# Performance work log

Measured on AMD Instinct MI355X. Metric: run time of the kernel, lower is better.

The kernel has to match this reference:

```python
import jax, jax.numpy as jnp
import numpy as np

ALPHA = 0.15
KSIZE = 5
EPS = 1e-6


def _minmax_norm(x):
    # x: [B,1,H,W]; per-sample min-max normalize, 0.5 if nearly constant
    mn = x.min(axis=(1, 2, 3), keepdims=True)
    mx = x.max(axis=(1, 2, 3), keepdims=True)
    denom = mx - mn
    safe = jnp.where(denom > EPS, denom, 1.0)
    return jnp.where(denom > EPS, (x - mn) / safe, 0.5)


def _saliency_map(images, out_hw):
    # grayscale via luma weights
    w = jnp.array([0.299, 0.587, 0.114], dtype=images.dtype).reshape(1, 3, 1, 1)
    gray = (images * w).sum(axis=1, keepdims=True)  # [B,1,H,W]
    kernel = jnp.ones((1, 1, KSIZE, KSIZE), dtype=gray.dtype) / (KSIZE * KSIZE)
    dn = ('NCHW', 'OIHW', 'NCHW')
    local_mean = jax.lax.conv_general_dilated(gray, kernel, (1, 1), 'SAME', dimension_numbers=dn)
    local_mean_sq = jax.lax.conv_general_dilated(gray ** 2, kernel, (1, 1), 'SAME', dimension_numbers=dn)
    local_var = jnp.maximum(local_mean_sq - local_mean ** 2, 0.0)
    sal = _minmax_norm(local_var)
    if sal.shape[-2:] != out_hw:
        sal = jax.image.resize(sal, (sal.shape[0], 1, out_hw[0], out_hw[1]), method='bilinear')
    return jax.lax.stop_gradient(sal)  # computed under no_grad / detached in torch


def setup_inputs() -> dict:
    key = jax.random.key(0)
    k1, k2 = jax.random.split(key)
    features = jax.random.normal(k1, (64, 512, 28, 28), dtype=jnp.float32)
    images = jax.random.uniform(k2, (64, 3, 224, 224), dtype=jnp.float32)
    return {"features": features, "images": images}


def reference(features, images):
    sal = _saliency_map(images, features.shape[-2:])  # [B,1,Hf,Wf]
    attn = jnp.sqrt((features ** 2).mean(axis=1, keepdims=True))  # [B,1,Hf,Wf]
    attn = _minmax_norm(attn)
    loss = jnp.mean((attn - sal) ** 2)
    return ALPHA * loss
```

## Files before the change

kernel.cpp:

```cpp
#include <hip/hip_runtime.h>
#include <math.h>

#define BATCH 64
#define HIMG 224
#define WIMG 224
#define IMGPLANE (HIMG*WIMG)
#define CF 512
#define HF 28
#define WF 28
#define POS (HF*WF)
#define ALPHA_C 0.15f
#define EPS_C 1e-6f

#define STRIPS 14
#define SROWS 16
#define GROWS 20
#define GCOLS 228
#define GSTR 229
#define VSTR 261

#define OFF_HRES 0
#define HRES_CNT (BATCH*HIMG*WF)
#define OFF_BMM (OFF_HRES + HRES_CNT)
#define OFF_AP  (OFF_BMM + BATCH*STRIPS*2)
#define OFF_LP  (OFF_AP + 2*BATCH*POS)

__global__ __launch_bounds__(256) void varh_k(const float* __restrict__ img,
                                              float* __restrict__ ws) {
    __shared__ float g[GROWS * GSTR];
    __shared__ float v[SROWS * VSTR];
    __shared__ float wred[8];
    int b = blockIdx.y, sy = blockIdx.x;
    int tid = threadIdx.x;
    int y0 = sy * SROWS;
    const float* imb = img + (size_t)b * 3 * IMGPLANE;

    for (int i = tid; i < GROWS * GCOLS; i += 256) {
        int gr = i / GCOLS, gc = i - gr * GCOLS;
        int gy = y0 - 2 + gr, gx = gc - 2;
        float u = 0.0f;
        if ((unsigned)gy < HIMG && (unsigned)gx < WIMG) {
            int o = gy * WIMG + gx;
            u = 0.299f * imb[o] + 0.587f * imb[IMGPLANE + o] + 0.114f * imb[2 * IMGPLANE + o];
        }
        g[gr * GSTR + gc] = u;
    }
    if (tid < SROWS * 8) {
        int r = tid >> 3, p = tid & 7;
        int jh = p + ((p < 4) ? 0 : 224);
        v[r * VSTR + jh + (jh >> 3)] = 0.0f;
    }
    __syncthreads();

    int r = tid >> 4, s = tid & 15;
    int x0 = 14 * s;
    const float* gr0 = g + r * GSTR;
    float c1[5], c2[5];
    #pragma unroll
    for (int m = 0; m < 5; m++) {
        float a = 0.0f, a2 = 0.0f;
        #pragma unroll
        for (int k = 0; k < 5; k++) {
            float u = gr0[k * GSTR + x0 + m];
            a += u; a2 += u * u;
        }
        c1[m] = a; c2[m] = a2;
    }
    float vmn = INFINITY, vmx = 0.0f;
    #pragma unroll
    for (int xi = 0; xi < 14; xi++) {
        int p = xi % 5;
        float s1 = c1[p], s2 = c2[p];
        #pragma unroll
        for (int m = 1; m < 5; m++) {
            s1 += c1[(p + m) % 5];
            s2 += c2[(p + m) % 5];
        }
        float m1 = s1 * 0.04f, m2 = s2 * 0.04f;
        float vv = fmaxf(m2 - m1 * m1, 0.0f);
        int jh = x0 + xi + 4;
        v[r * VSTR + jh + (jh >> 3)] = vv;
        vmn = fminf(vmn, vv); vmx = fmaxf(vmx, vv);
        if (xi < 13) {
            float a = 0.0f, a2 = 0.0f;
            #pragma unroll
            for (int k = 0; k < 5; k++) {
                float u = gr0[k * GSTR + x0 + xi + 5];
                a += u; a2 += u * u;
            }
            c1[p] = a; c2[p] = a2;
        }
    }
    #pragma unroll
    for (int o = 32; o > 0; o >>= 1) {
        vmn = fminf(vmn, __shfl_xor(vmn, o));
        vmx = fmaxf(vmx, __shfl_xor(vmx, o));
    }
    int w = tid >> 6;
    if ((tid & 63) == 0) { wred[w] = vmn; wred[4 + w] = vmx; }
    __syncthreads();
    if (tid == 0) {
        float mn = fminf(fminf(wred[0], wred[1]), fminf(wred[2], wred[3]));
        float mx = fmaxf(fmaxf(wred[4], wred[5]), fmaxf(wred[6], wred[7]));
        int blk = b * STRIPS + sy;
        ws[OFF_BMM + 2 * blk]     = mn;
        ws[OFF_BMM + 2 * blk + 1] = mx;
    }

    float* hb = ws + OFF_HRES + ((size_t)b * HIMG + y0) * WF;
    for (int idx = tid; idx < SROWS * WF; idx += 256) {
        int rr = idx / WF, i = idx - rr * WF;
        float acc = 0.0f, wsum = 0.0f;
        int j0 = 8 * i - 4;
        #pragma unroll
        for (int t = 0; t < 16; t++) {
            int j = j0 + t;
            float w_ = 8.0f - fabsf((float)t - 7.5f);
            int jh = j + 4;
            acc += w_ * v[rr * VSTR + jh + (jh >> 3)];
            if ((unsigned)j < WIMG) wsum += w_;
        }
        hb[idx] = acc / wsum;
    }
}

__global__ __launch_bounds__(256) void attn_k(const float* __restrict__ f,
                                              float* __restrict__ ws) {
    int p = blockIdx.x * 256 + threadIdx.x;
    int b = blockIdx.y, z = blockIdx.z;
    if (p >= POS) return;
    const float* fp = f + ((size_t)b * CF + (size_t)z * 256) * POS + p;
    float acc = 0.0f;
    #pragma unroll 16
    for (int c = 0; c < 256; c++) {
        float v = fp[(size_t)c * POS];
        acc += v * v;
    }
    ws[OFF_AP + ((size_t)z * BATCH + b) * POS + p] = acc;
}

__global__ __launch_bounds__(256) void fused_k(float* __restrict__ ws) {
    __shared__ float hres[HIMG][WF + 1];
    __shared__ float wred[4];
    __shared__ float s_mn, s_mx;
    int b = blockIdx.x;
    int tid = threadIdx.x;

    if (tid < 64) {
        float mn = INFINITY, mx = 0.0f;
        if (tid < STRIPS) {
            mn = ws[OFF_BMM + 2 * (b * STRIPS + tid)];
            mx = ws[OFF_BMM + 2 * (b * STRIPS + tid) + 1];
        }
        #pragma unroll
        for (int o = 8; o > 0; o >>= 1) {
            mn = fminf(mn, __shfl_down(mn, o));
            mx = fmaxf(mx, __shfl_down(mx, o));
        }
        if (tid == 0) { s_mn = mn; s_mx = mx; }
    }

    const float* hg = ws + OFF_HRES + (size_t)b * HIMG * WF;
    for (int i = tid; i < HIMG * WF; i += 256) {
        int y = i / WF, x = i - y * WF;
        hres[y][x] = hg[i];
    }
    __syncthreads();

    float vmn = s_mn, vmx = s_mx;
    float vden = vmx - vmn;
    bool vok = vden > EPS_C;

    const float* a0 = ws + OFF_AP + (size_t)b * POS;
    const float* a1 = ws + OFF_AP + ((size_t)BATCH + b) * POS;
    float salv[4], attnv[4];
    float amn = INFINITY, amx = -INFINITY;
    #pragma unroll
    for (int k = 0; k < 4; k++) {
        int idx = tid + 256 * k;
        salv[k] = 0.0f; attnv[k] = 0.0f;
        if (idx < POS) {
            int yo = idx / WF, x = idx - yo * WF;
            float acc = 0.0f, wsum = 0.0f;
            int j0 = 8 * yo - 4;
            #pragma unroll
            for (int t = 0; t < 16; t++) {
                int j = j0 + t;
                float w = 8.0f - fabsf((float)t - 7.5f);
                if ((unsigned)j < HIMG) { acc += w * hres[j][x]; wsum += w; }
            }
            float sraw = acc / wsum;
            salv[k] = vok ? (sraw - vmn) / vden : 0.5f;
            float a = sqrtf((a0[idx] + a1[idx]) * (1.0f / CF));
            attnv[k] = a;
            amn = fminf(amn, a); amx = fmaxf(amx, a);
        }
    }

    #pragma unroll
    for (int o = 32; o > 0; o >>= 1) {
        amn = fminf(amn, __shfl_xor(amn, o));
        amx = fmaxf(amx, __shfl_xor(amx, o));
    }
    int w = tid >> 6;
    if ((tid & 63) == 0) wred[w] = amn;
    __syncthreads();
    if (tid == 0) s_mn = fminf(fminf(wred[0], wred[1]), fminf(wred[2], wred[3]));
    __syncthreads();
    if ((tid & 63) == 0) wred[w] = amx;
    __syncthreads();
    if (tid == 0) s_mx = fmaxf(fmaxf(wred[0], wred[1]), fmaxf(wred[2], wred[3]));
    __syncthreads();
    amn = s_mn; amx = s_mx;
    float aden = amx - amn;
    bool aok = aden > EPS_C;

    float lsum = 0.0f;
    #pragma unroll
    for (int k = 0; k < 4; k++) {
        int idx = tid + 256 * k;
        if (idx < POS) {
            float an = aok ? (attnv[k] - amn) / aden : 0.5f;
            float d = an - salv[k];
            lsum += d * d;
        }
    }
    #pragma unroll
    for (int o = 32; o > 0; o >>= 1) lsum += __shfl_xor(lsum, o);
    if ((tid & 63) == 0) wred[w] = lsum;
    __syncthreads();
    if (tid == 0)
        ws[OFF_LP + b] = wred[0] + wred[1] + wred[2] + wred[3];
}

__global__ void final_k(const float* __restrict__ ws, float* __restrict__ out) {
    int t = threadIdx.x;
    float v = ws[OFF_LP + t];
    #pragma unroll
    for (int o = 32; o > 0; o >>= 1) v += __shfl_xor(v, o);
    if (t == 0) out[0] = v * (ALPHA_C / (float)(BATCH * POS));
}

extern "C" void kernel_launch(void* const* d_in, const int* in_sizes, int n_in,
                              void* d_out, int out_size, void* d_ws, size_t ws_size,
                              hipStream_t stream) {
    const float* features = (const float*)d_in[0];
    const float* images   = (const float*)d_in[1];
    float* ws  = (float*)d_ws;
    float* out = (float*)d_out;

    hipLaunchKernelGGL(varh_k,  dim3(STRIPS, BATCH), dim3(256), 0, stream, images, ws);
    hipLaunchKernelGGL(attn_k,  dim3(4, BATCH, 2),   dim3(256), 0, stream, features, ws);
    hipLaunchKernelGGL(fused_k, dim3(BATCH),         dim3(256), 0, stream, ws);
    hipLaunchKernelGGL(final_k, dim3(1),             dim3(64),  0, stream, ws, out);
}
```

Measured before the change: 196.2 us.

## Merge attention and variance kernels into one launch; fold final reduce via atomics

```diff
diff --git a/kernel.cpp b/kernel.cpp
--- a/kernel.cpp
+++ b/kernel.cpp
@@ -19,19 +19,46 @@
 #define GSTR 229
 #define VSTR 261
 
+#define NATTN 512
+#define NVARH (STRIPS*BATCH)
+
 #define OFF_HRES 0
 #define HRES_CNT (BATCH*HIMG*WF)
 #define OFF_BMM (OFF_HRES + HRES_CNT)
 #define OFF_AP  (OFF_BMM + BATCH*STRIPS*2)
-#define OFF_LP  (OFF_AP + 2*BATCH*POS)
-
-__global__ __launch_bounds__(256) void varh_k(const float* __restrict__ img,
-                                              float* __restrict__ ws) {
+#define OFF_ACC (OFF_AP + 2*BATCH*POS)
+#define OFF_CNT (OFF_ACC + 1)
+
+__global__ __launch_bounds__(256) void fat_k(const float* __restrict__ img,
+                                             const float* __restrict__ f,
+                                             float* __restrict__ ws) {
     __shared__ float g[GROWS * GSTR];
     __shared__ float v[SROWS * VSTR];
     __shared__ float wred[8];
-    int b = blockIdx.y, sy = blockIdx.x;
+    int bid = blockIdx.x;
     int tid = threadIdx.x;
+
+    if (bid < NATTN) {
+        if (bid == 0 && tid == 0) {
+            ws[OFF_ACC] = 0.0f;
+            ((unsigned*)ws)[OFF_CNT] = 0u;
+        }
+        int p = (bid & 3) * 256 + tid;
+        int b = (bid >> 2) & 63, z = bid >> 8;
+        if (p >= POS) return;
+        const float* fp = f + ((size_t)b * CF + (size_t)z * 256) * POS + p;
+        float acc = 0.0f;
+        #pragma unroll 16
+        for (int c = 0; c < 256; c++) {
+            float u = fp[(size_t)c * POS];
+            acc += u * u;
+        }
+        ws[OFF_AP + ((size_t)z * BATCH + b) * POS + p] = acc;
+        return;
+    }
+
+    int vb = bid - NATTN;
+    int b = vb / STRIPS, sy = vb - b * STRIPS;
     int y0 = sy * SROWS;
     const float* imb = img + (size_t)b * 3 * IMGPLANE;
 
@@ -124,22 +151,8 @@
     }
 }
 
-__global__ __launch_bounds__(256) void attn_k(const float* __restrict__ f,
-                                              float* __restrict__ ws) {
-    int p = blockIdx.x * 256 + threadIdx.x;
-    int b = blockIdx.y, z = blockIdx.z;
-    if (p >= POS) return;
-    const float* fp = f + ((size_t)b * CF + (size_t)z * 256) * POS + p;
-    float acc = 0.0f;
-    #pragma unroll 16
-    for (int c = 0; c < 256; c++) {
-        float v = fp[(size_t)c * POS];
-        acc += v * v;
-    }
-    ws[OFF_AP + ((size_t)z * BATCH + b) * POS + p] = acc;
-}
-
-__global__ __launch_bounds__(256) void fused_k(float* __restrict__ ws) {
+__global__ __launch_bounds__(256) void fused_k(float* __restrict__ ws,
+                                               float* __restrict__ out) {
     __shared__ float hres[HIMG][WF + 1];
     __shared__ float wred[4];
     __shared__ float s_mn, s_mx;
@@ -229,16 +242,17 @@
     for (int o = 32; o > 0; o >>= 1) lsum += __shfl_xor(lsum, o);
     if ((tid & 63) == 0) wred[w] = lsum;
     __syncthreads();
-    if (tid == 0)
-        ws[OFF_LP + b] = wred[0] + wred[1] + wred[2] + wred[3];
-}
-
-__global__ void final_k(const float* __restrict__ ws, float* __restrict__ out) {
-    int t = threadIdx.x;
-    float v = ws[OFF_LP + t];
-    #pragma unroll
-    for (int o = 32; o > 0; o >>= 1) v += __shfl_xor(v, o);
-    if (t == 0) out[0] = v * (ALPHA_C / (float)(BATCH * POS));
+
+    if (tid == 0) {
+        float part = wred[0] + wred[1] + wred[2] + wred[3];
+        atomicAdd(ws + OFF_ACC, part);
+        __threadfence();
+        unsigned old = atomicAdd((unsigned*)ws + OFF_CNT, 1u);
+        if (old == BATCH - 1) {
+            float tot = atomicAdd(ws + OFF_ACC, 0.0f);
+            out[0] = tot * (ALPHA_C / (float)(BATCH * POS));
+        }
+    }
 }
 
 extern "C" void kernel_launch(void* const* d_in, const int* in_sizes, int n_in,
@@ -249,8 +263,7 @@
     float* ws  = (float*)d_ws;
     float* out = (float*)d_out;
 
-    hipLaunchKernelGGL(varh_k,  dim3(STRIPS, BATCH), dim3(256), 0, stream, images, ws);
-    hipLaunchKernelGGL(attn_k,  dim3(4, BATCH, 2),   dim3(256), 0, stream, features, ws);
-    hipLaunchKernelGGL(fused_k, dim3(BATCH),         dim3(256), 0, stream, ws);
-    hipLaunchKernelGGL(final_k, dim3(1),             dim3(64),  0, stream, ws, out);
+    hipLaunchKernelGGL(fat_k,   dim3(NATTN + NVARH), dim3(256), 0, stream,
+                       images, features, ws);
+    hipLaunchKernelGGL(fused_k, dim3(BATCH),         dim3(256), 0, stream, ws, out);
 }
```

Result: no change. 195.7 us (-0.3%).
